# Kernel tuning notes

Measured on AMD Instinct MI355X. Metric: run time of the kernel, lower is better.

The kernel has to match this reference:

```python
import jax, jax.numpy as jnp
import numpy as np
from jax import lax

EPS = 1e-5
N_CROPS = 501
CROP_W = 500
RF = 65          # temporal receptive field
KS = 15          # conv1 kernel size
POOL = 3


def _bn(x, g, b, m, v, axis=1):
    shp = [1] * x.ndim
    shp[axis] = -1
    inv = g.reshape(shp) / jnp.sqrt(v.reshape(shp) + EPS)
    return (x - m.reshape(shp)) * inv + b.reshape(shp)


def setup_inputs() -> dict:
    key = jax.random.key(0)
    ks = jax.random.split(key, 16)
    B, C_IN, CH, T = 16, 1, 22, 1001
    F = 36
    OUT = 4
    FLAT = F * 43  # 1548 (corrected fc in_features; repo constant 504 is inconsistent)
    d = {
        "x": jax.random.normal(ks[0], (B, C_IN, CH, T), jnp.float32),
        # temporal conv [1,65]
        "w_t": jax.random.normal(ks[1], (F, 1, 1, RF), jnp.float32) * 0.1,
        "b_t": jax.random.normal(ks[2], (F,), jnp.float32) * 0.1,
        "bn_t_g": jax.random.uniform(ks[3], (F,), jnp.float32, 0.5, 1.5),
        "bn_t_b": jax.random.normal(ks[4], (F,), jnp.float32) * 0.1,
        "bn_t_m": jax.random.normal(ks[5], (F,), jnp.float32) * 0.1,
        "bn_t_v": jax.random.uniform(ks[6], (F,), jnp.float32, 0.5, 1.5),
        # spatial conv [22,1]
        "w_s": jax.random.normal(ks[7], (F, F, CH, 1), jnp.float32) * 0.05,
        "b_s": jax.random.normal(ks[8], (F,), jnp.float32) * 0.1,
        "bn_s_g": jax.random.uniform(ks[9], (F,), jnp.float32, 0.5, 1.5),
        "bn_s_b": jax.random.normal(ks[10], (F,), jnp.float32) * 0.1,
        "bn_s_m": jax.random.normal(ks[11], (F,), jnp.float32) * 0.1,
        "bn_s_v": jax.random.uniform(ks[12], (F,), jnp.float32, 0.5, 1.5),
        # conv1 [1,15] (as 1-D conv over time)
        "w_c": jax.random.normal(ks[13], (F, F, KS), jnp.float32) * 0.05,
        "b_c": jax.random.normal(ks[14], (F,), jnp.float32) * 0.1,
        "bn_c_g": jnp.ones((F,), jnp.float32),
        "bn_c_b": jnp.zeros((F,), jnp.float32),
        "bn_c_m": jnp.zeros((F,), jnp.float32),
        "bn_c_v": jnp.ones((F,), jnp.float32),
        # fc
        "w_fc": jax.random.normal(ks[15], (OUT, FLAT), jnp.float32) * 0.02,
        "b_fc": jnp.zeros((OUT,), jnp.float32),
    }
    return d


def reference(x, w_t, b_t, bn_t_g, bn_t_b, bn_t_m, bn_t_v,
              w_s, b_s, bn_s_g, bn_s_b, bn_s_m, bn_s_v,
              w_c, b_c, bn_c_g, bn_c_b, bn_c_m, bn_c_v,
              w_fc, b_fc):
    B = x.shape[0]
    F = w_t.shape[0]
    OUT = b_fc.shape[0]

    # temporal + spatial conv/BN/ELU are shift-invariant -> compute once over full T
    h = lax.conv_general_dilated(x, w_t, (1, 1), 'VALID',
                                 dimension_numbers=('NCHW', 'OIHW', 'NCHW'))
    h = h + b_t[None, :, None, None]                       # [B,36,22,937]
    h = jax.nn.elu(_bn(h, bn_t_g, bn_t_b, bn_t_m, bn_t_v))
    h = lax.conv_general_dilated(h, w_s, (1, 1), 'VALID',
                                 dimension_numbers=('NCHW', 'OIHW', 'NCHW'))
    h = h + b_s[None, :, None, None]                       # [B,36,1,937]
    h = jax.nn.elu(_bn(h, bn_s_g, bn_s_b, bn_s_m, bn_s_v))
    h = h[:, :, 0, :]                                      # [B,36,937]

    TW = CROP_W - RF + 1  # 436: temporal width of each crop after temporal conv

    def crop_logits(i):
        sl = lax.dynamic_slice_in_dim(h, i, TW, axis=2)    # [B,36,436]
        p1 = sl[:, :, :435].reshape(B, F, 145, POOL).mean(-1)  # avgpool1 -> [B,36,145]
        c = lax.conv_general_dilated(p1, w_c, (1,), 'VALID',
                                     dimension_numbers=('NCH', 'OIH', 'NCH'))
        c = c + b_c[None, :, None]                          # [B,36,131]
        c = jax.nn.elu(_bn(c, bn_c_g, bn_c_b, bn_c_m, bn_c_v))
        p2 = c[:, :, :129].reshape(B, F, 43, POOL).mean(-1)  # avgpool2 -> [B,36,43]
        flat = p2.reshape(B, -1)                            # [B,1548]
        return flat @ w_fc.T + b_fc                         # [B,OUT]

    def step(acc, i):
        return acc + crop_logits(i), None

    init = jnp.zeros((B, OUT), x.dtype)
    total, _ = lax.scan(step, init, jnp.arange(N_CROPS))
    return total / N_CROPS
```

## Files before the change

### kernel.cpp

```cpp
#include <hip/hip_runtime.h>

#define EPS 1e-5f
#define B 16
#define CH 22
#define T_IN 1001
#define F 36
#define RF 65
#define T1 937
#define FC 792
#define KW 99
#define UN 885
#define PS2 112
#define KS 15
#define GN 295
#define WN 129
#define M43 43
#define BF 576
#define FLAT 1548

#define H2_OFF  0
#define EP_OFF  539712
#define WTT_OFF 4617792
#define WST_OFF 4620132
#define WCT_OFF 4648644
#define BN_OFF  4668084
#define H1_OFF  4668352

__device__ __forceinline__ float elu_f(float v) {
    return v > 0.f ? v : (__expf(v) - 1.f);
}

__global__ __launch_bounds__(256) void k_prep(
    const float* __restrict__ w_t, const float* __restrict__ w_s,
    const float* __restrict__ w_c,
    const float* __restrict__ b_t, const float* __restrict__ g_t,
    const float* __restrict__ be_t,const float* __restrict__ m_t,
    const float* __restrict__ v_t,
    const float* __restrict__ b_s, const float* __restrict__ g_s,
    const float* __restrict__ be_s,const float* __restrict__ m_s,
    const float* __restrict__ v_s,
    const float* __restrict__ b_c, const float* __restrict__ g_c,
    const float* __restrict__ be_c,const float* __restrict__ m_c,
    const float* __restrict__ v_c, const float* __restrict__ b_fc,
    float* __restrict__ wtT, float* __restrict__ wsT,
    float* __restrict__ wcT, float* __restrict__ bnz,
    float* __restrict__ out)
{
    int i = blockIdx.x * 256 + threadIdx.x;
    if (i < F * RF)     { int k = i / F,  fi = i % F; wtT[i] = w_t[fi * RF + k]; }
    if (i < FC * F)     { int fc = i / F, fo = i % F; wsT[i] = w_s[fo * FC + fc]; }
    if (i < F * KS * F) { int fk = i / F, fo = i % F; int f = fk / KS, k = fk % KS;
                          wcT[i] = w_c[(fo * F + f) * KS + k]; }
    if (i < F) {
        float s1 = g_t[i] * rsqrtf(v_t[i] + EPS);
        bnz[i]          = s1;
        bnz[F + i]      = (b_t[i] - m_t[i]) * s1 + be_t[i];
        float s2 = g_s[i] * rsqrtf(v_s[i] + EPS);
        bnz[2 * F + i]  = s2;
        bnz[3 * F + i]  = (b_s[i] - m_s[i]) * s2 + be_s[i];
        float s3 = g_c[i] * rsqrtf(v_c[i] + EPS);
        bnz[4 * F + i]  = s3;
        bnz[5 * F + i]  = (b_c[i] - m_c[i]) * s3 + be_c[i];
    }
    if (i < B * 4) out[i] = b_fc[i & 3];
}

__global__ __launch_bounds__(256) void k_tconv(
    const float* __restrict__ x, const float* __restrict__ wtT,
    const float* __restrict__ bnz, float* __restrict__ h1,
    int t_base, int TS, int TSeff)
{
    const int tloc = blockIdx.x * 256 + threadIdx.x;
    const int b = blockIdx.z, ch = blockIdx.y;
    int t = t_base + tloc;
    int tc = t < (T1 - 1) ? t : (T1 - 1);
    const float* xp = x + (b * CH + ch) * T_IN + tc;

    float acc[F];
    #pragma unroll
    for (int j = 0; j < F; ++j) acc[j] = 0.f;

    #pragma unroll 4
    for (int kk = 0; kk < 16; ++kk) {
        float4 xv4 = *(const float4*)(xp + 4 * kk);
        const float* wr0 = wtT + (4 * kk + 0) * F;
        const float* wr1 = wtT + (4 * kk + 1) * F;
        const float* wr2 = wtT + (4 * kk + 2) * F;
        const float* wr3 = wtT + (4 * kk + 3) * F;
        #pragma unroll
        for (int j = 0; j < F; ++j) {
            acc[j] += xv4.x * wr0[j];
            acc[j] += xv4.y * wr1[j];
            acc[j] += xv4.z * wr2[j];
            acc[j] += xv4.w * wr3[j];
        }
    }
    {
        float xv = xp[64];
        const float* wr = wtT + 64 * F;
        #pragma unroll
        for (int j = 0; j < F; ++j) acc[j] += xv * wr[j];
    }

    if (t < T1 && tloc < TSeff) {
        #pragma unroll
        for (int j = 0; j < F; ++j) {
            float s1 = bnz[j], o1 = bnz[F + j];
            h1[((size_t)(b * F + j) * CH + ch) * TS + tloc] =
                elu_f(acc[j] * s1 + o1);
        }
    }
}

__global__ __launch_bounds__(512) void k_sconv(
    const float* __restrict__ h1, const float* __restrict__ wsT,
    const float* __restrict__ bnz, float* __restrict__ h2,
    int t_base, int TS, int TSeff)
{
    __shared__ float Ls[8 * F * 64];
    const int tid = threadIdx.x;
    const int lane = tid & 63;
    const int w = __builtin_amdgcn_readfirstlane(tid >> 6);
    const int b = blockIdx.y;
    const int tl0 = blockIdx.x * 64;
    int tl = tl0 + lane;
    int tlc = tl < (TSeff - 1) ? tl : (TSeff - 1);

    const float* hq = h1 + ((size_t)b * FC + w * KW) * TS + tlc;
    const float* wb = wsT + (w * KW) * F;

    float acc[F];
    #pragma unroll
    for (int j = 0; j < F; ++j) acc[j] = 0.f;

    #pragma unroll 11
    for (int fc = 0; fc < KW; ++fc) {
        float hv = hq[(size_t)fc * TS];
        const float* wr = wb + fc * F;
        #pragma unroll
        for (int j = 0; j < F; ++j) acc[j] += hv * wr[j];
    }

    #pragma unroll
    for (int j = 0; j < F; ++j) Ls[(w * F + j) * 64 + lane] = acc[j];
    __syncthreads();

    for (int i = tid; i < F * 64; i += 512) {
        float s = 0.f;
        #pragma unroll
        for (int wq = 0; wq < 8; ++wq) s += Ls[wq * (F * 64) + i];
        int fo = i >> 6;
        int tloc2 = tl0 + (i & 63);
        int tg = t_base + tloc2;
        if (tloc2 < TSeff) {
            float s2 = bnz[2 * F + fo], o2 = bnz[3 * F + fo];
            h2[(b * F + fo) * T1 + tg] = elu_f(s * s2 + o2);
        }
    }
}

__global__ __launch_bounds__(256) void k_qconv(
    const float* __restrict__ h2, const float* __restrict__ wcT,
    const float* __restrict__ bnz, float* __restrict__ A)
{
    __shared__ float Ps[F * PS2];
    const int tid = threadIdx.x;
    const int b = blockIdx.y;
    const int u0 = blockIdx.x * 64;
    const int lane = tid & 63;
    const int w = __builtin_amdgcn_readfirstlane(tid >> 6);

    for (int i = tid; i < F * PS2; i += 256) {
        int fl = i / PS2, j = i % PS2;
        const float* hr = h2 + (size_t)(b * F + fl) * T1;
        int s = u0 + j;
        int s0 = s     < T1 - 1 ? s     : T1 - 1;
        int s1 = s + 1 < T1 - 1 ? s + 1 : T1 - 1;
        int s2 = s + 2 < T1 - 1 ? s + 2 : T1 - 1;
        Ps[i] = (hr[s0] + hr[s1] + hr[s2]) * (1.f / 3.f);
    }
    __syncthreads();

    float acc[9];
    #pragma unroll
    for (int j = 0; j < 9; ++j) acc[j] = 0.f;

    const int fo0 = w * 9;
    for (int f = 0; f < F; ++f) {
        const int pb = f * PS2 + lane;
        #pragma unroll 5
        for (int k = 0; k < KS; ++k) {
            float pv = Ps[pb + 3 * k];
            const float* wr = wcT + (f * KS + k) * F + fo0;
            #pragma unroll
            for (int j = 0; j < 9; ++j) acc[j] += pv * wr[j];
        }
    }

    int u_g = u0 + lane;
    if (u_g < UN) {
        #pragma unroll
        for (int j = 0; j < 9; ++j) {
            int fo = fo0 + j;
            float sc = bnz[4 * F + fo], oc = bnz[5 * F + fo];
            A[((size_t)(b * F + fo)) * UN + u_g] = elu_f(acc[j] * sc + oc);
        }
    }
}

__global__ __launch_bounds__(256) void k_wins(
    const float* __restrict__ A, const float* __restrict__ w_fc,
    float* __restrict__ out)
{
    __shared__ float Es[UN];
    __shared__ float G[GN];
    __shared__ float Ws[WN];
    __shared__ float Sm[M43];
    const int tid = threadIdx.x;
    const int bf = blockIdx.x;
    const int b = bf / F, f = bf % F;
    for (int i = tid; i < UN; i += 256)
        Es[i] = A[(size_t)bf * UN + i];
    __syncthreads();
    for (int q = tid; q < GN; q += 256)
        G[q] = Es[3 * q] + Es[3 * q + 1] + Es[3 * q + 2];
    __syncthreads();
    if (tid < WN) {
        float a = 0.f;
        for (int q = tid; q < tid + 167; ++q) a += G[q];
        Ws[tid] = a;
    }
    __syncthreads();
    if (tid < M43)
        Sm[tid] = (Ws[3 * tid] + Ws[3 * tid + 1] + Ws[3 * tid + 2]) * (1.f / 3.f);
    __syncthreads();
    if (tid < 4) {
        const float* wr = w_fc + tid * FLAT + f * M43;
        float a = 0.f;
        #pragma unroll 43
        for (int m = 0; m < M43; ++m) a += Sm[m] * wr[m];
        atomicAdd(&out[b * 4 + tid], a * (1.f / 501.f));
    }
}

extern "C" void kernel_launch(void* const* d_in, const int* in_sizes, int n_in,
                              void* d_out, int out_size, void* d_ws, size_t ws_size,
                              hipStream_t stream) {
    const float* x    = (const float*)d_in[0];
    const float* w_t  = (const float*)d_in[1];
    const float* b_t  = (const float*)d_in[2];
    const float* g_t  = (const float*)d_in[3];
    const float* be_t = (const float*)d_in[4];
    const float* m_t  = (const float*)d_in[5];
    const float* v_t  = (const float*)d_in[6];
    const float* w_s  = (const float*)d_in[7];
    const float* b_s  = (const float*)d_in[8];
    const float* g_s  = (const float*)d_in[9];
    const float* be_s = (const float*)d_in[10];
    const float* m_s  = (const float*)d_in[11];
    const float* v_s  = (const float*)d_in[12];
    const float* w_c  = (const float*)d_in[13];
    const float* b_c  = (const float*)d_in[14];
    const float* g_c  = (const float*)d_in[15];
    const float* be_c = (const float*)d_in[16];
    const float* m_c  = (const float*)d_in[17];
    const float* v_c  = (const float*)d_in[18];
    const float* w_fc = (const float*)d_in[19];
    const float* b_fc = (const float*)d_in[20];

    float* ws  = (float*)d_ws;
    float* h2  = ws + H2_OFF;
    float* A   = ws + EP_OFF;
    float* wtT = ws + WTT_OFF;
    float* wsT = ws + WST_OFF;
    float* wcT = ws + WCT_OFF;
    float* bnz = ws + BN_OFF;
    float* h1  = ws + H1_OFF;
    float* out = (float*)d_out;

    long long availF = (long long)(ws_size / 4) - (long long)H1_OFF;
    long long tsl = availF / (B * FC);
    int TS;
    if (tsl >= T1) TS = T1;
    else { TS = (int)(tsl & ~63LL); if (TS < 64) TS = 64; }
    int nslab = (T1 + TS - 1) / TS;

    k_prep<<<dim3(112), 256, 0, stream>>>(
        w_t, w_s, w_c, b_t, g_t, be_t, m_t, v_t,
        b_s, g_s, be_s, m_s, v_s, b_c, g_c, be_c, m_c, v_c, b_fc,
        wtT, wsT, wcT, bnz, out);

    for (int sl = 0; sl < nslab; ++sl) {
        int t_base = sl * TS;
        int TSeff = T1 - t_base; if (TSeff > TS) TSeff = TS;
        k_tconv<<<dim3((TSeff + 255) / 256, CH, B), 256, 0, stream>>>(
            x, wtT, bnz, h1, t_base, TS, TSeff);
        k_sconv<<<dim3((TSeff + 63) / 64, B), 512, 0, stream>>>(
            h1, wsT, bnz, h2, t_base, TS, TSeff);
    }

    k_qconv<<<dim3(14, B), 256, 0, stream>>>(h2, wcT, bnz, A);
    k_wins<<<dim3(BF), 256, 0, stream>>>(A, w_fc, out);
}
```

Before: 199.2 us.

## Fuse temporal and spatial convs into one kernel, drop h1 buffer

Merges the temporal conv and spatial conv into a single 1024-thread kernel that stages the input in shared memory, computes h1 per channel in registers and accumulates the spatial conv directly, then reduces partial sums across waves through LDS. This removes the large h1 intermediate written to and read back from global memory, along with the slab loop. k_qconv is also reworked so each wave handles a subset of input filters for all outputs, followed by a tree reduction in shared memory. Only 15x16 blocks are launched for the fused kernel, so GPU occupancy may be low, and the 36-float accumulators raise register pressure.

```diff
diff --git a/kernel.cpp b/kernel.cpp
--- a/kernel.cpp
+++ b/kernel.cpp
@@ -8,9 +8,8 @@
 #define RF 65
 #define T1 937
 #define FC 792
-#define KW 99
 #define UN 885
-#define PS2 112
+#define PS3 112
 #define KS 15
 #define GN 295
 #define WN 129
@@ -19,12 +18,11 @@
 #define FLAT 1548
 
 #define H2_OFF  0
-#define EP_OFF  539712
+#define A_OFF   539712
 #define WTT_OFF 4617792
 #define WST_OFF 4620132
 #define WCT_OFF 4648644
 #define BN_OFF  4668084
-#define H1_OFF  4668352
 
 __device__ __forceinline__ float elu_f(float v) {
     return v > 0.f ? v : (__expf(v) - 1.f);
@@ -65,145 +63,191 @@
     if (i < B * 4) out[i] = b_fc[i & 3];
 }
 
-__global__ __launch_bounds__(256) void k_tconv(
-    const float* __restrict__ x, const float* __restrict__ wtT,
-    const float* __restrict__ bnz, float* __restrict__ h1,
-    int t_base, int TS, int TSeff)
+__global__ __launch_bounds__(1024) void k_fused(
+    const float* __restrict__ x, const float* __restrict__ w_t,
+    const float* __restrict__ wsT, const float* __restrict__ bnz,
+    float* __restrict__ h2)
 {
-    const int tloc = blockIdx.x * 256 + threadIdx.x;
-    const int b = blockIdx.z, ch = blockIdx.y;
-    int t = t_base + tloc;
-    int tc = t < (T1 - 1) ? t : (T1 - 1);
-    const float* xp = x + (b * CH + ch) * T_IN + tc;
+    __shared__ float xs[CH * 128];
+    __shared__ float comb[8][64][F];
+    const int tid  = threadIdx.x;
+    const int lane = tid & 63;
+    const int w = __builtin_amdgcn_readfirstlane(tid >> 6);
+    const int q = w >> 2;
+    const int g = w & 3;
+    const int b  = blockIdx.y;
+    const int t0 = blockIdx.x * 64;
+
+    for (int i = tid; i < CH * 128; i += 1024) {
+        int ch = i >> 7, j = i & 127;
+        int t = t0 + j; if (t > T_IN - 1) t = T_IN - 1;
+        xs[i] = x[(b * CH + ch) * T_IN + t];
+    }
+    __syncthreads();
+
+    const int ch0 = (q < 2) ? q * 6 : 12 + (q - 2) * 5;
+    const int nch = (q < 2) ? 6 : 5;
+    const int fi0 = g * 9;
 
     float acc[F];
     #pragma unroll
     for (int j = 0; j < F; ++j) acc[j] = 0.f;
 
-    #pragma unroll 4
-    for (int kk = 0; kk < 16; ++kk) {
-        float4 xv4 = *(const float4*)(xp + 4 * kk);
-        const float* wr0 = wtT + (4 * kk + 0) * F;
-        const float* wr1 = wtT + (4 * kk + 1) * F;
-        const float* wr2 = wtT + (4 * kk + 2) * F;
-        const float* wr3 = wtT + (4 * kk + 3) * F;
-        #pragma unroll
-        for (int j = 0; j < F; ++j) {
-            acc[j] += xv4.x * wr0[j];
-            acc[j] += xv4.y * wr1[j];
-            acc[j] += xv4.z * wr2[j];
-            acc[j] += xv4.w * wr3[j];
-        }
-    }
-    {
-        float xv = xp[64];
-        const float* wr = wtT + 64 * F;
-        #pragma unroll
-        for (int j = 0; j < F; ++j) acc[j] += xv * wr[j];
-    }
-
-    if (t < T1 && tloc < TSeff) {
-        #pragma unroll
-        for (int j = 0; j < F; ++j) {
-            float s1 = bnz[j], o1 = bnz[F + j];
-            h1[((size_t)(b * F + j) * CH + ch) * TS + tloc] =
-                elu_f(acc[j] * s1 + o1);
-        }
-    }
-}
-
-__global__ __launch_bounds__(512) void k_sconv(
-    const float* __restrict__ h1, const float* __restrict__ wsT,
-    const float* __restrict__ bnz, float* __restrict__ h2,
-    int t_base, int TS, int TSeff)
-{
-    __shared__ float Ls[8 * F * 64];
-    const int tid = threadIdx.x;
-    const int lane = tid & 63;
-    const int w = __builtin_amdgcn_readfirstlane(tid >> 6);
-    const int b = blockIdx.y;
-    const int tl0 = blockIdx.x * 64;
-    int tl = tl0 + lane;
-    int tlc = tl < (TSeff - 1) ? tl : (TSeff - 1);
-
-    const float* hq = h1 + ((size_t)b * FC + w * KW) * TS + tlc;
-    const float* wb = wsT + (w * KW) * F;
-
-    float acc[F];
-    #pragma unroll
-    for (int j = 0; j < F; ++j) acc[j] = 0.f;
-
-    #pragma unroll 11
-    for (int fc = 0; fc < KW; ++fc) {
-        float hv = hq[(size_t)fc * TS];
-        const float* wr = wb + fc * F;
-        #pragma unroll
-        for (int j = 0; j < F; ++j) acc[j] += hv * wr[j];
-    }
-
-    #pragma unroll
-    for (int j = 0; j < F; ++j) Ls[(w * F + j) * 64 + lane] = acc[j];
-    __syncthreads();
-
-    for (int i = tid; i < F * 64; i += 512) {
-        float s = 0.f;
-        #pragma unroll
-        for (int wq = 0; wq < 8; ++wq) s += Ls[wq * (F * 64) + i];
-        int fo = i >> 6;
-        int tloc2 = tl0 + (i & 63);
-        int tg = t_base + tloc2;
-        if (tloc2 < TSeff) {
-            float s2 = bnz[2 * F + fo], o2 = bnz[3 * F + fo];
-            h2[(b * F + fo) * T1 + tg] = elu_f(s * s2 + o2);
-        }
-    }
-}
-
-__global__ __launch_bounds__(256) void k_qconv(
+    for (int c = 0; c < nch; ++c) {
+        const int ch = ch0 + c;
+        const float* xr = xs + ch * 128 + lane;
+        const float* wt = w_t + fi0 * RF;
+
+        float h1a[9];
+        #pragma unroll
+        for (int j = 0; j < 9; ++j) h1a[j] = 0.f;
+
+        #pragma unroll
+        for (int k = 0; k < RF; ++k) {
+            float xv = xr[k];
+            #pragma unroll
+            for (int j = 0; j < 9; ++j)
+                h1a[j] += xv * wt[j * RF + k];
+        }
+        #pragma unroll
+        for (int j = 0; j < 9; ++j) {
+            float s1 = bnz[fi0 + j], o1 = bnz[F + fi0 + j];
+            h1a[j] = elu_f(h1a[j] * s1 + o1);
+        }
+        #pragma unroll
+        for (int j = 0; j < 9; ++j) {
+            const float* wr = wsT + ((fi0 + j) * CH + ch) * F;
+            float e = h1a[j];
+            #pragma unroll
+            for (int fo = 0; fo < F; ++fo)
+                acc[fo] += e * wr[fo];
+        }
+    }
+
+    for (int half = 8; half >= 1; half >>= 1) {
+        if (w >= half && w < 2 * half) {
+            float4* cb = (float4*)&comb[w - half][lane][0];
+            #pragma unroll
+            for (int j = 0; j < 9; ++j)
+                cb[j] = make_float4(acc[4*j], acc[4*j+1], acc[4*j+2], acc[4*j+3]);
+        }
+        __syncthreads();
+        if (w < half) {
+            const float4* cb = (const float4*)&comb[w][lane][0];
+            #pragma unroll
+            for (int j = 0; j < 9; ++j) {
+                float4 v = cb[j];
+                acc[4*j]   += v.x; acc[4*j+1] += v.y;
+                acc[4*j+2] += v.z; acc[4*j+3] += v.w;
+            }
+        }
+        __syncthreads();
+    }
+
+    if (w == 0) {
+        int t = t0 + lane;
+        if (t < T1) {
+            #pragma unroll
+            for (int fo = 0; fo < F; ++fo) {
+                float s2 = bnz[2 * F + fo], o2 = bnz[3 * F + fo];
+                h2[(b * F + fo) * T1 + t] = elu_f(acc[fo] * s2 + o2);
+            }
+        }
+    }
+}
+
+__global__ __launch_bounds__(768) void k_qconv(
     const float* __restrict__ h2, const float* __restrict__ wcT,
     const float* __restrict__ bnz, float* __restrict__ A)
 {
-    __shared__ float Ps[F * PS2];
-    const int tid = threadIdx.x;
-    const int b = blockIdx.y;
-    const int u0 = blockIdx.x * 64;
+    __shared__ float Ps[12][3][PS3];
+    __shared__ float comb[6][64][F];
+    const int tid  = threadIdx.x;
     const int lane = tid & 63;
     const int w = __builtin_amdgcn_readfirstlane(tid >> 6);
-
-    for (int i = tid; i < F * PS2; i += 256) {
-        int fl = i / PS2, j = i % PS2;
-        const float* hr = h2 + (size_t)(b * F + fl) * T1;
+    const int b  = blockIdx.y;
+    const int u0 = blockIdx.x * 64;
+    const int f0 = w * 3;
+
+    for (int i = lane; i < 3 * PS3; i += 64) {
+        int fl = i / PS3, j = i % PS3;
+        const float* hr = h2 + (size_t)(b * F + f0 + fl) * T1;
         int s = u0 + j;
         int s0 = s     < T1 - 1 ? s     : T1 - 1;
         int s1 = s + 1 < T1 - 1 ? s + 1 : T1 - 1;
         int s2 = s + 2 < T1 - 1 ? s + 2 : T1 - 1;
-        Ps[i] = (hr[s0] + hr[s1] + hr[s2]) * (1.f / 3.f);
-    }
-    __syncthreads();
-
-    float acc[9];
+        Ps[w][fl][j] = (hr[s0] + hr[s1] + hr[s2]) * (1.f / 3.f);
+    }
+
+    float acc[F];
     #pragma unroll
-    for (int j = 0; j < 9; ++j) acc[j] = 0.f;
-
-    const int fo0 = w * 9;
-    for (int f = 0; f < F; ++f) {
-        const int pb = f * PS2 + lane;
-        #pragma unroll 5
+    for (int j = 0; j < F; ++j) acc[j] = 0.f;
+
+    #pragma unroll
+    for (int fl = 0; fl < 3; ++fl) {
+        #pragma unroll
         for (int k = 0; k < KS; ++k) {
-            float pv = Ps[pb + 3 * k];
-            const float* wr = wcT + (f * KS + k) * F + fo0;
-            #pragma unroll
-            for (int j = 0; j < 9; ++j) acc[j] += pv * wr[j];
-        }
-    }
-
-    int u_g = u0 + lane;
-    if (u_g < UN) {
-        #pragma unroll
-        for (int j = 0; j < 9; ++j) {
-            int fo = fo0 + j;
-            float sc = bnz[4 * F + fo], oc = bnz[5 * F + fo];
-            A[((size_t)(b * F + fo)) * UN + u_g] = elu_f(acc[j] * sc + oc);
+            float pv = Ps[w][fl][lane + 3 * k];
+            const float* wr = wcT + ((f0 + fl) * KS + k) * F;
+            #pragma unroll
+            for (int fo = 0; fo < F; ++fo) acc[fo] += pv * wr[fo];
+        }
+    }
+
+    if (w >= 6) {
+        float4* cb = (float4*)&comb[w - 6][lane][0];
+        #pragma unroll
+        for (int j = 0; j < 9; ++j)
+            cb[j] = make_float4(acc[4*j], acc[4*j+1], acc[4*j+2], acc[4*j+3]);
+    }
+    __syncthreads();
+    if (w < 6) {
+        const float4* cb = (const float4*)&comb[w][lane][0];
+        #pragma unroll
+        for (int j = 0; j < 9; ++j) {
+            float4 v = cb[j];
+            acc[4*j] += v.x; acc[4*j+1] += v.y; acc[4*j+2] += v.z; acc[4*j+3] += v.w;
+        }
+    }
+    __syncthreads();
+    if (w >= 3 && w < 6) {
+        float4* cb = (float4*)&comb[w - 3][lane][0];
+        #pragma unroll
+        for (int j = 0; j < 9; ++j)
+            cb[j] = make_float4(acc[4*j], acc[4*j+1], acc[4*j+2], acc[4*j+3]);
+    }
+    __syncthreads();
+    if (w < 3) {
+        const float4* cb = (const float4*)&comb[w][lane][0];
+        #pragma unroll
+        for (int j = 0; j < 9; ++j) {
+            float4 v = cb[j];
+            acc[4*j] += v.x; acc[4*j+1] += v.y; acc[4*j+2] += v.z; acc[4*j+3] += v.w;
+        }
+    }
+    __syncthreads();
+    if (w == 1 || w == 2) {
+        float4* cb = (float4*)&comb[w - 1][lane][0];
+        #pragma unroll
+        for (int j = 0; j < 9; ++j)
+            cb[j] = make_float4(acc[4*j], acc[4*j+1], acc[4*j+2], acc[4*j+3]);
+    }
+    __syncthreads();
+    if (w == 0) {
+        #pragma unroll
+        for (int j = 0; j < 9; ++j) {
+            float4 v0 = ((const float4*)&comb[0][lane][0])[j];
+            float4 v1 = ((const float4*)&comb[1][lane][0])[j];
+            acc[4*j]   += v0.x + v1.x; acc[4*j+1] += v0.y + v1.y;
+            acc[4*j+2] += v0.z + v1.z; acc[4*j+3] += v0.w + v1.w;
+        }
+        int u_g = u0 + lane;
+        if (u_g < UN) {
+            #pragma unroll
+            for (int fo = 0; fo < F; ++fo) {
+                float sc = bnz[4 * F + fo], oc = bnz[5 * F + fo];
+                A[((size_t)(b * F + fo)) * UN + u_g] = elu_f(acc[fo] * sc + oc);
+            }
         }
     }
 }
@@ -270,35 +314,19 @@
 
     float* ws  = (float*)d_ws;
     float* h2  = ws + H2_OFF;
-    float* A   = ws + EP_OFF;
+    float* A   = ws + A_OFF;
     float* wtT = ws + WTT_OFF;
     float* wsT = ws + WST_OFF;
     float* wcT = ws + WCT_OFF;
     float* bnz = ws + BN_OFF;
-    float* h1  = ws + H1_OFF;
     float* out = (float*)d_out;
-
-    long long availF = (long long)(ws_size / 4) - (long long)H1_OFF;
-    long long tsl = availF / (B * FC);
-    int TS;
-    if (tsl >= T1) TS = T1;
-    else { TS = (int)(tsl & ~63LL); if (TS < 64) TS = 64; }
-    int nslab = (T1 + TS - 1) / TS;
 
     k_prep<<<dim3(112), 256, 0, stream>>>(
         w_t, w_s, w_c, b_t, g_t, be_t, m_t, v_t,
         b_s, g_s, be_s, m_s, v_s, b_c, g_c, be_c, m_c, v_c, b_fc,
         wtT, wsT, wcT, bnz, out);
 
-    for (int sl = 0; sl < nslab; ++sl) {
-        int t_base = sl * TS;
-        int TSeff = T1 - t_base; if (TSeff > TS) TSeff = TS;
-        k_tconv<<<dim3((TSeff + 255) / 256, CH, B), 256, 0, stream>>>(
-            x, wtT, bnz, h1, t_base, TS, TSeff);
-        k_sconv<<<dim3((TSeff + 63) / 64, B), 512, 0, stream>>>(
-            h1, wsT, bnz, h2, t_base, TS, TSeff);
-    }
-
-    k_qconv<<<dim3(14, B), 256, 0, stream>>>(h2, wcT, bnz, A);
+    k_fused<<<dim3(15, B), 1024, 0, stream>>>(x, w_t, wsT, bnz, h2);
+    k_qconv<<<dim3(14, B), 768, 0, stream>>>(h2, wcT, bnz, A);
     k_wins<<<dim3(BF), 256, 0, stream>>>(A, w_fc, out);
 }
```

Measured after the change: 242.3 us. +21.7%, slower.
